# Kernel tuning notes

Measured on AMD Instinct MI355X. Metric: run time of the kernel, lower is better.

## Reference

```python
import jax, jax.numpy as jnp
import numpy as np

EMBED_DIM = 1024
NUM_HEADS = 16
HEAD_DIM = EMBED_DIM // NUM_HEADS
SCALE = HEAD_DIM ** -0.5
BATCH, SEQ = 8, 1024


def setup_inputs() -> dict:
    key = jax.random.key(0)
    ks = jax.random.split(key, 5)
    x = jax.random.normal(ks[0], (BATCH, SEQ, EMBED_DIM), dtype=jnp.float32)
    # nn.Linear params: weight [out, in], bias [out]
    w_qkv = jax.random.normal(ks[1], (3 * EMBED_DIM, EMBED_DIM), dtype=jnp.float32) * (EMBED_DIM ** -0.5)
    b_qkv = jax.random.normal(ks[2], (3 * EMBED_DIM,), dtype=jnp.float32) * 0.02
    w_proj = jax.random.normal(ks[3], (EMBED_DIM, EMBED_DIM), dtype=jnp.float32) * (EMBED_DIM ** -0.5)
    b_proj = jax.random.normal(ks[4], (EMBED_DIM,), dtype=jnp.float32) * 0.02
    return {"x": x, "w_qkv": w_qkv, "b_qkv": b_qkv, "w_proj": w_proj, "b_proj": b_proj}


def reference(x, w_qkv, b_qkv, w_proj, b_proj):
    B, N, E = x.shape
    # qkv projection: [B, N, 3E]
    qkv = jnp.einsum('bne,fe->bnf', x, w_qkv) + b_qkv
    qkv = qkv.reshape(B, N, 3, NUM_HEADS, HEAD_DIM)
    qkv = jnp.transpose(qkv, (2, 0, 3, 1, 4))  # [3, B, H, N, D]
    q, k, v = qkv[0], qkv[1], qkv[2]
    # naive full attention (faithful to source): [B, H, N, N]
    scores = jnp.einsum('bhqd,bhkd->bhqk', q, k) * SCALE
    probs = jax.nn.softmax(scores, axis=-1)
    attn = jnp.einsum('bhqk,bhkd->bhqd', probs, v)
    attn = jnp.transpose(attn, (0, 2, 1, 3)).reshape(B, N, E)
    out = jnp.einsum('bne,fe->bnf', attn, w_proj) + b_proj
    return out
```

## Files before the change

### kernel.cpp

```cpp
#include <hip/hip_runtime.h>
#include <cstdint>

typedef _Float16 f16;
typedef _Float16 f16x8 __attribute__((ext_vector_type(8)));
typedef _Float16 f16x4 __attribute__((ext_vector_type(4)));
typedef _Float16 f16x2 __attribute__((ext_vector_type(2)));
typedef float    f32x4 __attribute__((ext_vector_type(4)));
typedef float    f32x16 __attribute__((ext_vector_type(16)));
typedef unsigned int uint;
typedef uint     uintx2 __attribute__((ext_vector_type(2)));

#define NB   8
#define SEQL 1024
#define EMB  1024
#define NH   16
#define HD   64
#define MR   (NB*SEQL)
#define BHND ((size_t)NB*NH*SEQL*HD)

static __device__ __forceinline__ void gload16(const void* g, void* l) {
  __builtin_amdgcn_global_load_lds(
      (const __attribute__((address_space(1))) char*)(uintptr_t)g,
      (__attribute__((address_space(3))) char*)(uintptr_t)l,
      16, 0, 0);
}

static __device__ __forceinline__ uint packf16(float a, float b) {
  f16x2 h; h[0] = (f16)a; h[1] = (f16)b;
  return __builtin_bit_cast(uint, h);
}

__global__ __launch_bounds__(256) void cvt_f32_f16(const float* __restrict__ src,
                                                   f16* __restrict__ dst, int n4) {
  int i = blockIdx.x * 256 + threadIdx.x;
  if (i >= n4) return;
  float4 v = ((const float4*)src)[i];
  f16x4 h;
  h[0] = (f16)v.x; h[1] = (f16)v.y; h[2] = (f16)v.z; h[3] = (f16)v.w;
  *(f16x4*)(dst + (size_t)i * 4) = h;
}

template<int NTOT, int MODE>
__global__ __launch_bounds__(256, 2) void gemm_bt(const f16* __restrict__ A,
                                                  const f16* __restrict__ Bt,
                                                  const float* __restrict__ bias,
                                                  void* __restrict__ outp) {
  __shared__ char smem[32768];
  const int t = threadIdx.x;
  const int w = t >> 6, lane = t & 63;
  const int lg = lane >> 4, lc = lane & 15;
  const int m0 = blockIdx.x * 128;
  const int n0 = blockIdx.y * 128;
  const int wr = w >> 1, wc = w & 1;

  f32x4 acc[4][4];
#pragma unroll
  for (int i = 0; i < 4; ++i)
#pragma unroll
    for (int j = 0; j < 4; ++j) acc[i][j] = (f32x4){0.f, 0.f, 0.f, 0.f};

  const char* Ab = (const char*)A + (size_t)m0 * 2048;
  const char* Bb = (const char*)Bt + (size_t)n0 * 2048;

  for (int k0 = 0; k0 < 1024; k0 += 64) {
#pragma unroll
    for (int f = 0; f < 4; ++f) {
      const int ci = f * 4 + w;
      const int x = ci * 1024 + lane * 16;
      const int row = x >> 7;
      const int col = (x & 127) ^ ((row & 7) << 4);
      gload16(Ab + (size_t)row * 2048 + k0 * 2 + col, smem + ci * 1024);
      gload16(Bb + (size_t)row * 2048 + k0 * 2 + col, smem + 16384 + ci * 1024);
    }
    __syncthreads();

#pragma unroll
    for (int kk = 0; kk < 2; ++kk) {
      f16x8 af[4], bf[4];
#pragma unroll
      for (int i = 0; i < 4; ++i) {
        const int ra = wr * 64 + i * 16 + lc;
        int ba = ra * 128 + kk * 64 + lg * 16;
        ba ^= (ra & 7) << 4;
        af[i] = *(const f16x8*)(smem + ba);
        const int rb = wc * 64 + i * 16 + lc;
        int bb = rb * 128 + kk * 64 + lg * 16;
        bb ^= (rb & 7) << 4;
        bf[i] = *(const f16x8*)(smem + 16384 + bb);
      }
#pragma unroll
      for (int i = 0; i < 4; ++i)
#pragma unroll
        for (int j = 0; j < 4; ++j)
          acc[i][j] = __builtin_amdgcn_mfma_f32_16x16x32_f16(af[i], bf[j], acc[i][j], 0, 0, 0);
    }
    __syncthreads();
  }

  float biasv[4];
#pragma unroll
  for (int j = 0; j < 4; ++j) biasv[j] = bias[n0 + wc * 64 + j * 16 + lc];

  if (MODE == 1) {
    float* Out = (float*)outp;
#pragma unroll
    for (int i = 0; i < 4; ++i)
#pragma unroll
      for (int j = 0; j < 4; ++j) {
        const int colL = n0 + wc * 64 + j * 16 + lc;
#pragma unroll
        for (int r = 0; r < 4; ++r) {
          const int row = m0 + wr * 64 + i * 16 + lg * 4 + r;
          Out[(size_t)row * NTOT + colL] = acc[i][j][r] + biasv[j];
        }
      }
  } else {
    f16* qkv = (f16*)outp;
#pragma unroll
    for (int i = 0; i < 4; ++i) {
      const int rbase = m0 + wr * 64 + i * 16 + lg * 4;
#pragma unroll
      for (int j = 0; j < 4; ++j) {
        const int colL = n0 + wc * 64 + j * 16 + lc;
        const int which = colL >> 10;
        const int e = colL & 1023;
        const int h = e >> 6, d = e & 63;
#pragma unroll
        for (int r = 0; r < 4; ++r) {
          const int rr = rbase + r;
          const int b = rr >> 10, n = rr & 1023;
          qkv[(size_t)which * BHND + ((size_t)(b * NH + h) * SEQL + n) * HD + d] =
              (f16)(acc[i][j][r] + biasv[j]);
        }
      }
    }
  }
}

__global__ __launch_bounds__(256) void transpose_v(const f16* __restrict__ V,
                                                   f16* __restrict__ Vt) {
  __shared__ f16 tile[64 * 72];
  const int bid = blockIdx.x;
  const int bh = bid >> 4, nt = bid & 15;
  const int t = threadIdx.x;
  const int r = t >> 2, c0 = (t & 3) * 16;
  const f16* src = V + ((size_t)bh * SEQL + nt * 64 + r) * HD + c0;
  f16x8 a0 = *(const f16x8*)src;
  f16x8 a1 = *(const f16x8*)(src + 8);
#pragma unroll
  for (int e = 0; e < 8; ++e) {
    tile[(c0 + e) * 72 + r] = a0[e];
    tile[(c0 + 8 + e) * 72 + r] = a1[e];
  }
  __syncthreads();
  f16* dst = Vt + ((size_t)bh * HD + r) * SEQL + nt * 64 + c0;
  *(f16x8*)dst = *(const f16x8*)&tile[r * 72 + c0];
  *(f16x8*)(dst + 8) = *(const f16x8*)&tile[r * 72 + c0 + 8];
}

__global__ __launch_bounds__(256, 2) void attn_fwd(const f16* __restrict__ Q,
                                                   const f16* __restrict__ Kh,
                                                   const f16* __restrict__ Vt,
                                                   f16* __restrict__ Oh) {
  __shared__ uint4 Kl4[512];
  __shared__ uint4 Vl4[512];
  char* Kl = (char*)Kl4;
  char* Vl = (char*)Vl4;

  const int bid = blockIdx.x;
  const int bh = bid & 127;
  const int qb = bid >> 7;
  const int t = threadIdx.x;
  const int w = t >> 6, lane = t & 63;
  const int l31 = lane & 31, hi = lane >> 5;

  const char* kbp = (const char*)Kh + (size_t)bh * 131072;
  const char* vbp = (const char*)Vt + (size_t)bh * 131072;

  const f16* qp = Q + ((size_t)bh * SEQL + qb * 128 + w * 32 + l31) * HD;
  f16x8 qf[4];
#pragma unroll
  for (int dc = 0; dc < 4; ++dc) {
    f16x8 v = *(const f16x8*)(qp + dc * 16 + hi * 8);
#pragma unroll
    for (int e = 0; e < 8; ++e) v[e] = v[e] * (f16)0.125f;
    qf[dc] = v;
  }

  f32x16 acc0, acc1;
#pragma unroll
  for (int i = 0; i < 16; ++i) { acc0[i] = 0.f; acc1[i] = 0.f; }
  float m = -1e30f, l = 0.f;

  for (int kt = 0; kt < 16; ++kt) {
#pragma unroll
    for (int f = 0; f < 2; ++f) {
      const int ci = w * 2 + f;
      const int x = ci * 1024 + lane * 16;
      const int row = x >> 7;
      const int col = (x & 127) ^ ((row & 7) << 4);
      gload16(kbp + (size_t)(kt * 64 + row) * 128 + col, Kl + ci * 1024);
      gload16(vbp + (size_t)row * 2048 + kt * 128 + col, Vl + ci * 1024);
    }
    __syncthreads();

    f32x16 s0, s1;
#pragma unroll
    for (int i = 0; i < 16; ++i) { s0[i] = 0.f; s1[i] = 0.f; }
#pragma unroll
    for (int dc = 0; dc < 4; ++dc) {
      const int cb = dc * 32 + hi * 16;
      const int a0 = (l31 * 128 + cb) ^ ((l31 & 7) << 4);
      const int a1 = ((l31 + 32) * 128 + cb) ^ ((l31 & 7) << 4);
      f16x8 kf0 = *(const f16x8*)(Kl + a0);
      f16x8 kf1 = *(const f16x8*)(Kl + a1);
      s0 = __builtin_amdgcn_mfma_f32_32x32x16_f16(kf0, qf[dc], s0, 0, 0, 0);
      s1 = __builtin_amdgcn_mfma_f32_32x32x16_f16(kf1, qf[dc], s1, 0, 0, 0);
    }

    float v[32];
#pragma unroll
    for (int i = 0; i < 16; ++i) { v[i] = s0[i]; v[16 + i] = s1[i]; }
#pragma unroll
    for (int st = 16; st >= 1; st >>= 1)
#pragma unroll
      for (int i = 0; i < st; ++i) v[i] = fmaxf(v[i], v[i + st]);
    const float mx = fmaxf(v[0], __shfl_xor(v[0], 32));

    if (__any(mx > m + 8.f)) {
      const float nm = fmaxf(m, mx);
      const float al = __expf(m - nm);
      m = nm;
      l *= al;
      acc0 *= al;
      acc1 *= al;
    }

    float p[32];
#pragma unroll
    for (int i = 0; i < 16; ++i) {
      p[i] = __expf(s0[i] - m);
      p[16 + i] = __expf(s1[i] - m);
    }
    float ts[32];
#pragma unroll
    for (int i = 0; i < 32; ++i) ts[i] = p[i];
#pragma unroll
    for (int st = 16; st >= 1; st >>= 1)
#pragma unroll
      for (int i = 0; i < st; ++i) ts[i] += ts[i + st];
    const float rs = ts[0] + __shfl_xor(ts[0], 32);
    l += rs;

    uint wk[16];
#pragma unroll
    for (int i = 0; i < 16; ++i) wk[i] = packf16(p[2 * i], p[2 * i + 1]);

#pragma unroll
    for (int ksub = 0; ksub < 2; ++ksub)
#pragma unroll
      for (int kh = 0; kh < 2; ++kh) {
        const int b0 = ksub * 8 + kh * 4;
        uintx2 r02 = __builtin_amdgcn_permlane32_swap(wk[b0 + 0], wk[b0 + 2], false, false);
        uintx2 r13 = __builtin_amdgcn_permlane32_swap(wk[b0 + 1], wk[b0 + 3], false, false);
        union { uint u[4]; f16x8 v; } fb;
        fb.u[0] = r02[0];
        fb.u[1] = r13[0];
        fb.u[2] = r02[1];
        fb.u[3] = r13[1];
        const int cb = ksub * 64 + kh * 32 + hi * 16;
        const int av0 = (l31 * 128 + cb) ^ ((l31 & 7) << 4);
        const int av1 = ((l31 + 32) * 128 + cb) ^ ((l31 & 7) << 4);
        f16x8 vf0 = *(const f16x8*)(Vl + av0);
        f16x8 vf1 = *(const f16x8*)(Vl + av1);
        acc0 = __builtin_amdgcn_mfma_f32_32x32x16_f16(vf0, fb.v, acc0, 0, 0, 0);
        acc1 = __builtin_amdgcn_mfma_f32_32x32x16_f16(vf1, fb.v, acc1, 0, 0, 0);
      }
    __syncthreads();
  }

  const int b = bh >> 4, h = bh & 15;
  const float inv = 1.f / l;
  f16* ob = Oh + ((size_t)(b * SEQL) + qb * 128 + w * 32 + l31) * EMB + h * 64;
#pragma unroll
  for (int g = 0; g < 4; ++g) {
    f16x4 o0, o1;
#pragma unroll
    for (int e = 0; e < 4; ++e) {
      o0[e] = (f16)(acc0[g * 4 + e] * inv);
      o1[e] = (f16)(acc1[g * 4 + e] * inv);
    }
    *(f16x4*)(ob + g * 8 + hi * 4) = o0;
    *(f16x4*)(ob + 32 + g * 8 + hi * 4) = o1;
  }
}

extern "C" void kernel_launch(void* const* d_in, const int* in_sizes, int n_in,
                              void* d_out, int out_size, void* d_ws, size_t ws_size,
                              hipStream_t stream) {
  (void)in_sizes; (void)n_in; (void)out_size; (void)ws_size;
  const float* x      = (const float*)d_in[0];
  const float* w_qkv  = (const float*)d_in[1];
  const float* b_qkv  = (const float*)d_in[2];
  const float* w_proj = (const float*)d_in[3];
  const float* b_proj = (const float*)d_in[4];
  char* ws = (char*)d_ws;

  const size_t XH = 0;
  const size_t WQ = 16777216;
  const size_t WP = 23068672;
  const size_t QH = 25165824;
  const size_t KH = 41943040;
  const size_t VH = 58720256;
  const size_t VT = 0;
  const size_t AH = VH;

  f16* xh  = (f16*)(ws + XH);
  f16* wqh = (f16*)(ws + WQ);
  f16* wph = (f16*)(ws + WP);

  cvt_f32_f16<<<(MR * EMB / 4 + 255) / 256, 256, 0, stream>>>(x, xh, MR * EMB / 4);
  cvt_f32_f16<<<(3 * EMB * EMB / 4 + 255) / 256, 256, 0, stream>>>(w_qkv, wqh, 3 * EMB * EMB / 4);
  cvt_f32_f16<<<(EMB * EMB / 4 + 255) / 256, 256, 0, stream>>>(w_proj, wph, EMB * EMB / 4);

  gemm_bt<3072, 0><<<dim3(64, 24), 256, 0, stream>>>(xh, wqh, b_qkv, (void*)(ws + QH));

  transpose_v<<<NB * NH * (SEQL / 64), 256, 0, stream>>>((const f16*)(ws + VH), (f16*)(ws + VT));

  attn_fwd<<<NB * NH * 8, 256, 0, stream>>>((const f16*)(ws + QH),
                                            (const f16*)(ws + KH),
                                            (const f16*)(ws + VT),
                                            (f16*)(ws + AH));

  gemm_bt<1024, 1><<<dim3(64, 8), 256, 0, stream>>>((const f16*)(ws + AH), wph, b_proj, d_out);
}
```

Baseline: 250.7 us.

## Fuse V transpose into QKV GEMM epilogue and merge conversion kernels

The QKV GEMM epilogue now writes V directly in transposed [B,H,D,N] layout using 4-wide half stores, so the separate transpose kernel and its extra read/write pass over V are gone. The three fp32-to-fp16 conversion launches are merged into one kernel that picks its source by index range. The transposed V stores are strided across lanes, which may coalesce poorly. The workspace layout is reshuffled so the attention output reuses the dead x buffer.

Measured after the change: 230.8 us. 7.9% less time.

```diff
diff --git a/kernel.cpp b/kernel.cpp
--- a/kernel.cpp
+++ b/kernel.cpp
@@ -30,21 +30,29 @@
   return __builtin_bit_cast(uint, h);
 }
 
-__global__ __launch_bounds__(256) void cvt_f32_f16(const float* __restrict__ src,
-                                                   f16* __restrict__ dst, int n4) {
-  int i = blockIdx.x * 256 + threadIdx.x;
-  if (i >= n4) return;
-  float4 v = ((const float4*)src)[i];
+__global__ __launch_bounds__(256) void cvt_all(const float* __restrict__ x,
+                                               const float* __restrict__ wq,
+                                               const float* __restrict__ wp,
+                                               f16* __restrict__ xh,
+                                               f16* __restrict__ wqh,
+                                               f16* __restrict__ wph) {
+  const int i = blockIdx.x * 256 + threadIdx.x;
+  const float* src; f16* dst; int j;
+  if (i < 2097152)      { src = x;  dst = xh;  j = i; }
+  else if (i < 2883584) { src = wq; dst = wqh; j = i - 2097152; }
+  else                  { src = wp; dst = wph; j = i - 2883584; }
+  float4 v = ((const float4*)src)[j];
   f16x4 h;
   h[0] = (f16)v.x; h[1] = (f16)v.y; h[2] = (f16)v.z; h[3] = (f16)v.w;
-  *(f16x4*)(dst + (size_t)i * 4) = h;
+  *(f16x4*)(dst + (size_t)j * 4) = h;
 }
 
 template<int NTOT, int MODE>
 __global__ __launch_bounds__(256, 2) void gemm_bt(const f16* __restrict__ A,
                                                   const f16* __restrict__ Bt,
                                                   const float* __restrict__ bias,
-                                                  void* __restrict__ outp) {
+                                                  void* __restrict__ outp,
+                                                  void* __restrict__ outp2) {
   __shared__ char smem[32768];
   const int t = threadIdx.x;
   const int w = t >> 6, lane = t & 63;
@@ -115,47 +123,35 @@
         }
       }
   } else {
-    f16* qkv = (f16*)outp;
+    f16* qk = (f16*)outp;
+    f16* vt = (f16*)outp2;
 #pragma unroll
     for (int i = 0; i < 4; ++i) {
       const int rbase = m0 + wr * 64 + i * 16 + lg * 4;
+      const int bb = rbase >> 10, nb = rbase & 1023;
 #pragma unroll
       for (int j = 0; j < 4; ++j) {
         const int colL = n0 + wc * 64 + j * 16 + lc;
         const int which = colL >> 10;
         const int e = colL & 1023;
         const int h = e >> 6, d = e & 63;
-#pragma unroll
-        for (int r = 0; r < 4; ++r) {
-          const int rr = rbase + r;
-          const int b = rr >> 10, n = rr & 1023;
-          qkv[(size_t)which * BHND + ((size_t)(b * NH + h) * SEQL + n) * HD + d] =
-              (f16)(acc[i][j][r] + biasv[j]);
+        if (which == 2) {
+          f16x4 vv;
+#pragma unroll
+          for (int r = 0; r < 4; ++r) vv[r] = (f16)(acc[i][j][r] + biasv[j]);
+          *(f16x4*)(vt + ((size_t)(bb * NH + h) * HD + d) * SEQL + nb) = vv;
+        } else {
+#pragma unroll
+          for (int r = 0; r < 4; ++r) {
+            const int rr = rbase + r;
+            const int b = rr >> 10, n = rr & 1023;
+            qk[(size_t)which * BHND + ((size_t)(b * NH + h) * SEQL + n) * HD + d] =
+                (f16)(acc[i][j][r] + biasv[j]);
+          }
         }
       }
     }
   }
-}
-
-__global__ __launch_bounds__(256) void transpose_v(const f16* __restrict__ V,
-                                                   f16* __restrict__ Vt) {
-  __shared__ f16 tile[64 * 72];
-  const int bid = blockIdx.x;
-  const int bh = bid >> 4, nt = bid & 15;
-  const int t = threadIdx.x;
-  const int r = t >> 2, c0 = (t & 3) * 16;
-  const f16* src = V + ((size_t)bh * SEQL + nt * 64 + r) * HD + c0;
-  f16x8 a0 = *(const f16x8*)src;
-  f16x8 a1 = *(const f16x8*)(src + 8);
-#pragma unroll
-  for (int e = 0; e < 8; ++e) {
-    tile[(c0 + e) * 72 + r] = a0[e];
-    tile[(c0 + 8 + e) * 72 + r] = a1[e];
-  }
-  __syncthreads();
-  f16* dst = Vt + ((size_t)bh * HD + r) * SEQL + nt * 64 + c0;
-  *(f16x8*)dst = *(const f16x8*)&tile[r * 72 + c0];
-  *(f16x8*)(dst + 8) = *(const f16x8*)&tile[r * 72 + c0 + 8];
 }
 
 __global__ __launch_bounds__(256, 2) void attn_fwd(const f16* __restrict__ Q,
@@ -311,26 +307,23 @@
   const size_t WP = 23068672;
   const size_t QH = 25165824;
   const size_t KH = 41943040;
-  const size_t VH = 58720256;
-  const size_t VT = 0;
-  const size_t AH = VH;
+  const size_t VT = 58720256;
+  const size_t AH = 0;
 
   f16* xh  = (f16*)(ws + XH);
   f16* wqh = (f16*)(ws + WQ);
   f16* wph = (f16*)(ws + WP);
 
-  cvt_f32_f16<<<(MR * EMB / 4 + 255) / 256, 256, 0, stream>>>(x, xh, MR * EMB / 4);
-  cvt_f32_f16<<<(3 * EMB * EMB / 4 + 255) / 256, 256, 0, stream>>>(w_qkv, wqh, 3 * EMB * EMB / 4);
-  cvt_f32_f16<<<(EMB * EMB / 4 + 255) / 256, 256, 0, stream>>>(w_proj, wph, EMB * EMB / 4);
-
-  gemm_bt<3072, 0><<<dim3(64, 24), 256, 0, stream>>>(xh, wqh, b_qkv, (void*)(ws + QH));
-
-  transpose_v<<<NB * NH * (SEQL / 64), 256, 0, stream>>>((const f16*)(ws + VH), (f16*)(ws + VT));
+  cvt_all<<<12288, 256, 0, stream>>>(x, w_qkv, w_proj, xh, wqh, wph);
+
+  gemm_bt<3072, 0><<<dim3(64, 24), 256, 0, stream>>>(xh, wqh, b_qkv,
+                                                     (void*)(ws + QH), (void*)(ws + VT));
 
   attn_fwd<<<NB * NH * 8, 256, 0, stream>>>((const f16*)(ws + QH),
                                             (const f16*)(ws + KH),
                                             (const f16*)(ws + VT),
                                             (f16*)(ws + AH));
 
-  gemm_bt<1024, 1><<<dim3(64, 8), 256, 0, stream>>>((const f16*)(ws + AH), wph, b_proj, d_out);
-}
+  gemm_bt<1024, 1><<<dim3(64, 8), 256, 0, stream>>>((const f16*)(ws + AH), wph, b_proj,
+                                                    d_out, nullptr);
+}
```
